# Performance work log

Measured on AMD Instinct MI355X. Metric: run time of the kernel, lower is better.

The kernel has to match this reference:

```python
import jax, jax.numpy as jnp
import numpy as np

B, C, H, W = 4, 64, 512, 512


def setup_inputs() -> dict:
    key = jax.random.key(0)
    k1, k2, k3 = jax.random.split(key, 3)
    z = jax.random.uniform(k1, (B, C, H, W), dtype=jnp.float32)      # gate in (0,1)
    h_tilde = jax.random.normal(k2, (B, C, H, W), dtype=jnp.float32)  # candidate state
    h0 = jax.random.normal(k3, (B, C, 1, W), dtype=jnp.float32)       # initial state row
    return {"z": z, "h_tilde": h_tilde, "h0": h0}


def reference(z, h_tilde, h0):
    # GruDirection2d with dh=1, dw=0 (forward_h): linear recurrence along H
    #   h[t] = z[t] * h_tilde[t] + (1 - z[t]) * h[t-1],  h[-1] = h0
    # Expressed as a single lax.scan over the H axis; each step is a fused
    # elementwise update on a [B, C, W] slice.
    zs = jnp.moveaxis(z, 2, 0)        # [H, B, C, W]
    hs = jnp.moveaxis(h_tilde, 2, 0)  # [H, B, C, W]

    def step(carry, inp):
        zt, ht = inp
        h = zt * ht + (1.0 - zt) * carry
        return h, h

    _, out = jax.lax.scan(step, h0[:, :, 0, :], (zs, hs))
    return jnp.moveaxis(out, 0, 2)    # [B, C, H, W]
```

## Files before the change

kernel.cpp:

```cpp
#include <hip/hip_runtime.h>


constexpr int Bc = 4;
constexpr int Cc = 64;
constexpr int Hc = 512;
constexpr int Wc = 512;

__global__ __launch_bounds__(256) void gru_h_scan(const float* __restrict__ z,
                                                  const float* __restrict__ ht,
                                                  const float* __restrict__ h0,
                                                  float* __restrict__ out) {
    constexpr int W2 = Wc / 2;
    const int cid = blockIdx.x * blockDim.x + threadIdx.x;
    const int bc = cid / W2;
    const int w2 = cid - bc * W2;

    const size_t plane = (size_t)bc * Hc * Wc;
    const size_t col = (size_t)w2;

    float2 h = reinterpret_cast<const float2*>(h0)[(size_t)bc * W2 + col];

    const float2* zp = reinterpret_cast<const float2*>(z) + plane / 2 + col;
    const float2* hp = reinterpret_cast<const float2*>(ht) + plane / 2 + col;
    float2* op = reinterpret_cast<float2*>(out) + plane / 2 + col;

#pragma unroll 8
    for (int t = 0; t < Hc; ++t) {
        const size_t off = (size_t)t * W2;
        float2 zt = zp[off];
        float2 cd = hp[off];
        h.x = fmaf(zt.x, cd.x, (1.0f - zt.x) * h.x);
        h.y = fmaf(zt.y, cd.y, (1.0f - zt.y) * h.y);
        op[off] = h;
    }
}

extern "C" void kernel_launch(void* const* d_in, const int* in_sizes, int n_in,
                              void* d_out, int out_size, void* d_ws, size_t ws_size,
                              hipStream_t stream) {
    const float* z = (const float*)d_in[0];
    const float* h_tilde = (const float*)d_in[1];
    const float* h0 = (const float*)d_in[2];
    float* out = (float*)d_out;

    const int n_chains2 = Bc * Cc * (Wc / 2);
    const int block = 256;
    const int grid = n_chains2 / block;
    gru_h_scan<<<grid, block, 0, stream>>>(z, h_tilde, h0, out);
}
```

Baseline: 157.2 us.

## Use one column per thread with nontemporal stores and deeper unroll

Each thread now handles a single scalar column instead of a float2 pair, which doubles the thread count to raise memory-level parallelism across the sequential H recurrence. The unroll factor goes from 8 to 16 so more independent loads are in flight per thread, and output writes use nontemporal stores to avoid polluting cache with streaming data. The trade-off is narrower per-thread loads (4 bytes instead of 8) and more register pressure from the larger unroll.

```diff
diff --git a/kernel.cpp b/kernel.cpp
--- a/kernel.cpp
+++ b/kernel.cpp
@@ -10,28 +10,25 @@
                                                   const float* __restrict__ ht,
                                                   const float* __restrict__ h0,
                                                   float* __restrict__ out) {
-    constexpr int W2 = Wc / 2;
     const int cid = blockIdx.x * blockDim.x + threadIdx.x;
-    const int bc = cid / W2;
-    const int w2 = cid - bc * W2;
+    const int bc = cid / Wc;
+    const int w = cid - bc * Wc;
 
-    const size_t plane = (size_t)bc * Hc * Wc;
-    const size_t col = (size_t)w2;
+    const size_t base = (size_t)bc * Hc * Wc + w;
 
-    float2 h = reinterpret_cast<const float2*>(h0)[(size_t)bc * W2 + col];
+    float h = h0[(size_t)bc * Wc + w];
 
-    const float2* zp = reinterpret_cast<const float2*>(z) + plane / 2 + col;
-    const float2* hp = reinterpret_cast<const float2*>(ht) + plane / 2 + col;
-    float2* op = reinterpret_cast<float2*>(out) + plane / 2 + col;
+    const float* zp = z + base;
+    const float* hp = ht + base;
+    float* op = out + base;
 
-#pragma unroll 8
+#pragma unroll 16
     for (int t = 0; t < Hc; ++t) {
-        const size_t off = (size_t)t * W2;
-        float2 zt = zp[off];
-        float2 cd = hp[off];
-        h.x = fmaf(zt.x, cd.x, (1.0f - zt.x) * h.x);
-        h.y = fmaf(zt.y, cd.y, (1.0f - zt.y) * h.y);
-        op[off] = h;
+        const size_t off = (size_t)t * Wc;
+        const float zt = zp[off];
+        const float cd = hp[off];
+        h = fmaf(zt, cd, (1.0f - zt) * h);
+        __builtin_nontemporal_store(h, op + off);
     }
 }
 
@@ -43,8 +40,8 @@
     const float* h0 = (const float*)d_in[2];
     float* out = (float*)d_out;
 
-    const int n_chains2 = Bc * Cc * (Wc / 2);
+    const int n_chains = Bc * Cc * Wc;
     const int block = 256;
-    const int grid = n_chains2 / block;
+    const int grid = n_chains / block;
     gru_h_scan<<<grid, block, 0, stream>>>(z, h_tilde, h0, out);
 }
```

Measured after the change: 152.1 us. -3.2%, faster.
